# Performance work log

Measured on AMD Instinct MI355X. Metric: run time of the kernel, lower is better.

The kernel has to match this reference:

```python
import jax, jax.numpy as jnp
import numpy as np

B, T, L = 64, 256, 64          # batch, time steps, num_links
H = 128                        # hidden_size
E = 524288                     # num edges
N = B * T                      # nodes seen by GCNConv
IN = L + L * L                 # 4160: concat of link features + flattened distance matrix
OUT = 12 * L                   # fc output size
NUM_LSTM = 2


def setup_inputs() -> dict:
    key = jax.random.key(0)
    ks = jax.random.split(key, 24)
    inp = {
        "x": jax.random.normal(ks[0], (B, T, L), jnp.float32),
        "distance": jax.random.uniform(ks[1], (L, L), jnp.float32),
        "edge_index": jax.random.randint(ks[2], (2, E), 0, N, jnp.int64),
    }
    # GCN layer params (PyG GCNConv: lin weight [in,out] acting as x @ W, bias after aggregation)
    dims = [IN, H, H, H]
    for i in range(3):
        s = 1.0 / np.sqrt(dims[i])
        inp[f"gcn_W{i}"] = jax.random.normal(ks[3 + 2 * i], (dims[i], H), jnp.float32) * s
        inp[f"gcn_b{i}"] = jnp.zeros((H,), jnp.float32)
    # LSTM params, torch layout: W_ih [4H, Hin], W_hh [4H, H], gate order i,f,g,o
    s = 1.0 / np.sqrt(H)
    for l in range(NUM_LSTM):
        inp[f"Wih{l}"] = jax.random.normal(ks[10 + 4 * l], (4 * H, H), jnp.float32) * s
        inp[f"Whh{l}"] = jax.random.normal(ks[11 + 4 * l], (4 * H, H), jnp.float32) * s
        inp[f"bih{l}"] = jax.random.normal(ks[12 + 4 * l], (4 * H,), jnp.float32) * s
        inp[f"bhh{l}"] = jax.random.normal(ks[13 + 4 * l], (4 * H,), jnp.float32) * s
    inp["fc_W"] = jax.random.normal(ks[20], (OUT, H), jnp.float32) * s
    inp["fc_b"] = jnp.zeros((OUT,), jnp.float32)
    return inp


def _gcn(x, W, b, src, dst):
    # GCNConv with add_self_loops=True: out = D^-1/2 (A+I) D^-1/2 (x W) + b
    h = x @ W
    deg = jnp.ones((N,), h.dtype).at[dst].add(1.0)  # in-degree + self loop
    dinv = jax.lax.rsqrt(deg)
    norm = dinv[src] * dinv[dst]                    # [E]
    agg = jnp.zeros_like(h).at[dst].add(h[src] * norm[:, None])
    agg = agg + h * (dinv * dinv)[:, None]          # self-loop term
    return agg + b


def _lstm_layer(xs, Wih, Whh, bih, bhh):
    # xs: [T, B, Hin]
    bias = bih + bhh

    def step(carry, xt):
        h, c = carry
        g = xt @ Wih.T + h @ Whh.T + bias
        i, f, gg, o = jnp.split(g, 4, axis=-1)
        c = jax.nn.sigmoid(f) * c + jax.nn.sigmoid(i) * jnp.tanh(gg)
        h = jax.nn.sigmoid(o) * jnp.tanh(c)
        return (h, c), h

    h0 = jnp.zeros((xs.shape[1], H), xs.dtype)
    _, ys = jax.lax.scan(step, (h0, h0), xs)
    return ys


def reference(x, distance, gcn_W0, gcn_b0, gcn_W1, gcn_b1, gcn_W2, gcn_b2,
              Wih0, Whh0, bih0, bhh0, Wih1, Whh1, bih1, bhh1, fc_W, fc_b,
              edge_index):
    src, dst = edge_index[0], edge_index[1]
    xf = x.reshape(N, L)
    dist_flat = jnp.broadcast_to(distance.reshape(1, L * L), (N, L * L))
    feat = jnp.concatenate([xf, dist_flat], axis=1)  # [N, IN]
    for W, b in ((gcn_W0, gcn_b0), (gcn_W1, gcn_b1), (gcn_W2, gcn_b2)):
        feat = jax.nn.relu(_gcn(feat, W, b, src, dst))
    seq = feat.reshape(B, T, H).transpose(1, 0, 2)   # [T, B, H]
    seq = _lstm_layer(seq, Wih0, Whh0, bih0, bhh0)
    seq = _lstm_layer(seq, Wih1, Whh1, bih1, bhh1)
    last = seq[-1]                                   # [B, H]
    out = last @ fc_W.T + fc_b                       # [B, OUT]
    return out.reshape(B, 12, L)
```

## Files before the change

kernel.cpp:

```cpp
#include <hip/hip_runtime.h>
#include <hip/hip_bf16.h>
#include <cstdint>
#include <cstddef>

#define NB 64
#define NT 256
#define NL 64
#define NH 128
#define NN 16384
#define NE 524288
#define NG 512
#define NOUT 768


__global__ __launch_bounds__(256) void k_transpose(const float* __restrict__ W,
                                                   float* __restrict__ Wt,
                                                   int K, int Nout) {
  int i = blockIdx.x * 256 + threadIdx.x;
  if (i < K * Nout) {
    int k = i / Nout, n = i % Nout;
    Wt[n * K + k] = W[i];
  }
}

__global__ __launch_bounds__(256) void k_dvec(const float* __restrict__ dist,
                                              const float* __restrict__ W0,
                                              float* __restrict__ dvec) {
  __shared__ float red[256];
  int j = blockIdx.x;
  int t = threadIdx.x;
  float acc = 0.f;
  for (int m = t; m < 4096; m += 256)
    acc += dist[m] * W0[(size_t)(64 + m) * 128 + j];
  red[t] = acc;
  __syncthreads();
  for (int off = 128; off > 0; off >>= 1) {
    if (t < off) red[t] += red[t + off];
    __syncthreads();
  }
  if (t == 0) dvec[j] = red[0];
}

__global__ __launch_bounds__(256) void k_count(const int* __restrict__ dst,
                                               int* __restrict__ counts) {
  int i = blockIdx.x * 256 + threadIdx.x;
  atomicAdd(&counts[dst[i]], 1);
}

__global__ __launch_bounds__(256) void k_dinv(const int* __restrict__ counts,
                                              float* __restrict__ dinv) {
  int n = blockIdx.x * 256 + threadIdx.x;
  dinv[n] = rsqrtf((float)counts[n] + 1.0f);
}

__global__ __launch_bounds__(1024) void k_scan(const int* __restrict__ counts,
                                               int* __restrict__ rowstart) {
  __shared__ int part[1024];
  int t = threadIdx.x;
  int base = t * 16;
  int local[16];
  int s = 0;
#pragma unroll
  for (int i = 0; i < 16; i++) { local[i] = s; s += counts[base + i]; }
  part[t] = s;
  __syncthreads();
  for (int off = 1; off < 1024; off <<= 1) {
    int v = (t >= off) ? part[t - off] : 0;
    __syncthreads();
    part[t] += v;
    __syncthreads();
  }
  int prefix = (t == 0) ? 0 : part[t - 1];
#pragma unroll
  for (int i = 0; i < 16; i++) rowstart[base + i] = prefix + local[i];
  if (t == 1023) rowstart[16384] = part[1023];
}

__global__ __launch_bounds__(256) void k_fill(const int* __restrict__ src,
                                              const int* __restrict__ dst,
                                              const int* __restrict__ rowstart,
                                              int* __restrict__ fill,
                                              const float* __restrict__ dinv,
                                              int2* __restrict__ csr) {
  int e = blockIdx.x * 256 + threadIdx.x;
  int sN = src[e], dN = dst[e];
  int pos = rowstart[dN] + atomicAdd(&fill[dN], 1);
  csr[pos] = make_int2(sN, __float_as_int(dinv[sN] * dinv[dN]));
}

template <int K, bool RELU, bool PERMC = false>
__global__ __launch_bounds__(256) void k_gemm_abt(const float* __restrict__ A,
                                                  const float* __restrict__ Bm,
                                                  const float* __restrict__ bias0,
                                                  const float* __restrict__ bias1,
                                                  float* __restrict__ C, int Nn) {
  __shared__ float As[64][K];
  __shared__ float Bs[64][K];
  const int tid = threadIdx.x;
  const int bm = blockIdx.x, bn = blockIdx.y;
  const int VPR = K / 4;
  for (int i = tid; i < 64 * VPR; i += 256) {
    int r = i / VPR, c = i % VPR;
    int xr = (r >> 2) & 7;
    float4 q = *(const float4*)(A + (size_t)(bm * 64 + r) * K + c * 4);
    *(float4*)&As[r][(c ^ xr) * 4] = q;
  }
  for (int i = tid; i < 64 * VPR; i += 256) {
    int r = i / VPR, c = i % VPR;
    int xr = (r >> 2) & 7;
    float4 q = *(const float4*)(Bm + (size_t)(bn * 64 + r) * K + c * 4);
    *(float4*)&Bs[r][(c ^ xr) * 4] = q;
  }
  __syncthreads();
  const int tr = (tid >> 4) << 2;
  const int tc = (tid & 15) << 2;
  const int axor = (tr >> 2) & 7;
  const int bxor = (tc >> 2) & 7;
  float acc[4][4] = {};
#pragma unroll 2
  for (int k4 = 0; k4 < VPR; k4++) {
    int ka = (k4 ^ axor) * 4;
    int kb = (k4 ^ bxor) * 4;
    float4 a0 = *(const float4*)&As[tr + 0][ka];
    float4 a1 = *(const float4*)&As[tr + 1][ka];
    float4 a2 = *(const float4*)&As[tr + 2][ka];
    float4 a3 = *(const float4*)&As[tr + 3][ka];
    float4 b0 = *(const float4*)&Bs[tc + 0][kb];
    float4 b1 = *(const float4*)&Bs[tc + 1][kb];
    float4 b2 = *(const float4*)&Bs[tc + 2][kb];
    float4 b3 = *(const float4*)&Bs[tc + 3][kb];
#define DOT4(i2, j2, av, bv)                                                   \
    acc[i2][j2] = fmaf(av.x, bv.x, acc[i2][j2]);                               \
    acc[i2][j2] = fmaf(av.y, bv.y, acc[i2][j2]);                               \
    acc[i2][j2] = fmaf(av.z, bv.z, acc[i2][j2]);                               \
    acc[i2][j2] = fmaf(av.w, bv.w, acc[i2][j2]);
    DOT4(0, 0, a0, b0) DOT4(0, 1, a0, b1) DOT4(0, 2, a0, b2) DOT4(0, 3, a0, b3)
    DOT4(1, 0, a1, b0) DOT4(1, 1, a1, b1) DOT4(1, 2, a1, b2) DOT4(1, 3, a1, b3)
    DOT4(2, 0, a2, b0) DOT4(2, 1, a2, b1) DOT4(2, 2, a2, b2) DOT4(2, 3, a2, b3)
    DOT4(3, 0, a3, b0) DOT4(3, 1, a3, b1) DOT4(3, 2, a3, b2) DOT4(3, 3, a3, b3)
#undef DOT4
  }
#pragma unroll
  for (int i2 = 0; i2 < 4; i2++) {
    int row = bm * 64 + tr + i2;
#pragma unroll
    for (int j2 = 0; j2 < 4; j2++) {
      int col = bn * 64 + tc + j2;
      float v = acc[i2][j2];
      if (bias0) v += bias0[col];
      if (bias1) v += bias1[col];
      if (RELU) v = fmaxf(v, 0.f);
      int colw = PERMC ? ((col & 127) * 4 + (col >> 7)) : col;
      C[(size_t)row * Nn + colw] = v;
    }
  }
}

__global__ __launch_bounds__(256) void k_agg(const float* __restrict__ h,
                                             const int* __restrict__ rowstart,
                                             const int2* __restrict__ csr,
                                             const float* __restrict__ dinv,
                                             const float* __restrict__ bias,
                                             float* __restrict__ out) {
  int node = blockIdx.x * 4 + (threadIdx.x >> 6);
  int lane = threadIdx.x & 63;
  int s = rowstart[node], e = rowstart[node + 1];
  const float2* h2 = (const float2*)h;
  float ax = 0.f, ay = 0.f;
  int p = s;
  for (; p + 3 < e; p += 4) {
    int2 pk0 = csr[p];
    int2 pk1 = csr[p + 1];
    int2 pk2 = csr[p + 2];
    int2 pk3 = csr[p + 3];
    float2 hv0 = h2[(size_t)pk0.x * 64 + lane];
    float2 hv1 = h2[(size_t)pk1.x * 64 + lane];
    float2 hv2 = h2[(size_t)pk2.x * 64 + lane];
    float2 hv3 = h2[(size_t)pk3.x * 64 + lane];
    float w0 = __int_as_float(pk0.y);
    float w1 = __int_as_float(pk1.y);
    float w2 = __int_as_float(pk2.y);
    float w3 = __int_as_float(pk3.y);
    ax = fmaf(hv0.x, w0, ax); ay = fmaf(hv0.y, w0, ay);
    ax = fmaf(hv1.x, w1, ax); ay = fmaf(hv1.y, w1, ay);
    ax = fmaf(hv2.x, w2, ax); ay = fmaf(hv2.y, w2, ay);
    ax = fmaf(hv3.x, w3, ax); ay = fmaf(hv3.y, w3, ay);
  }
  for (; p < e; p++) {
    int2 pk0 = csr[p];
    float2 hv0 = h2[(size_t)pk0.x * 64 + lane];
    float w0 = __int_as_float(pk0.y);
    ax = fmaf(hv0.x, w0, ax); ay = fmaf(hv0.y, w0, ay);
  }
  float di = dinv[node];
  float sw = di * di;
  float2 hs = h2[(size_t)node * 64 + lane];
  float2 bv = ((const float2*)bias)[lane];
  ax = fmaf(hs.x, sw, ax) + bv.x;
  ay = fmaf(hs.y, sw, ay) + bv.y;
  float2 o;
  o.x = fmaxf(ax, 0.f);
  o.y = fmaxf(ay, 0.f);
  ((float2*)out)[(size_t)node * 64 + lane] = o;
}


template <int CTRL>
__device__ __forceinline__ float dppadd(float x) {
  int r = __builtin_amdgcn_update_dpp(0, __float_as_int(x), CTRL, 0xF, 0xF, true);
  return x + __int_as_float(r);
}

__device__ __forceinline__ float sigf(float x) {
  return 1.f / (1.f + __expf(-x));
}
__device__ __forceinline__ float tanhf_fast(float x) {
  return 1.f - 2.f / (__expf(2.f * x) + 1.f);
}

typedef float f4v __attribute__((ext_vector_type(4)));

template <bool LAST_ONLY>
__global__ __launch_bounds__(512)
__attribute__((amdgpu_waves_per_eu(2, 2)))
void k_lstm7(const float* __restrict__ pre,
             const float* __restrict__ Whh,
             float* __restrict__ yout) {
  __shared__ float hbuf[2][128];
  const int tid = threadIdx.x;
  const int b = blockIdx.x;
  const int c4 = tid & 3;
  const int u = tid >> 2;

  int hidx[8];
#pragma unroll
  for (int j = 0; j < 8; j++) hidx[j] = c4 * 8 + (((u & 7) + 2 * c4 + j) & 7);

#define DECLW(g, j) \
  f4v W##g##_##j = *(const f4v*)(Whh + (size_t)((g)*128 + u) * 128 + hidx[j] * 4);
#define DECLW_ROW(g) \
  DECLW(g, 0) DECLW(g, 1) DECLW(g, 2) DECLW(g, 3) \
  DECLW(g, 4) DECLW(g, 5) DECLW(g, 6) DECLW(g, 7)
  DECLW_ROW(0) DECLW_ROW(1) DECLW_ROW(2) DECLW_ROW(3)
#undef DECLW_ROW
#undef DECLW

  if (tid < 128) hbuf[0][tid] = 0.f;
  float cs = 0.f;
  const float* preb = pre + (size_t)b * NT * NG + tid;
  float pcur = preb[0];
  float* ybase = LAST_ONLY ? (yout + (size_t)b * NH + u)
                           : (yout + (size_t)b * NT * NH + u);
  __syncthreads();

#define PINW(g) \
  asm volatile("" : "+v"(W##g##_0), "+v"(W##g##_1), "+v"(W##g##_2), "+v"(W##g##_3)); \
  asm volatile("" : "+v"(W##g##_4), "+v"(W##g##_5), "+v"(W##g##_6), "+v"(W##g##_7));

#define FMA_J(j)                                                               \
  {                                                                            \
    f4v hv = hp[hidx[j]];                                                      \
    a0 = __builtin_elementwise_fma(W0_##j, hv, a0);                            \
    a1 = __builtin_elementwise_fma(W1_##j, hv, a1);                            \
    a2 = __builtin_elementwise_fma(W2_##j, hv, a2);                            \
    a3 = __builtin_elementwise_fma(W3_##j, hv, a3);                            \
  }

#define LSTM_STEP(CUR, NXT, T)                                                 \
  {                                                                            \
    int tn = (T) + 1; if (tn > NT - 1) tn = NT - 1;                            \
    float pnext = preb[(size_t)tn * NG];                                       \
    const f4v* hp = (const f4v*)&hbuf[CUR][0];                                 \
    f4v a0 = {0.f, 0.f, 0.f, 0.f}, a1 = a0, a2 = a0, a3 = a0;                  \
    FMA_J(0) FMA_J(1) FMA_J(2) FMA_J(3)                                        \
    FMA_J(4) FMA_J(5) FMA_J(6) FMA_J(7)                                        \
    float s0 = (a0.x + a0.y) + (a0.z + a0.w) + ((c4 == 0) ? pcur : 0.f);       \
    float s1 = (a1.x + a1.y) + (a1.z + a1.w) + ((c4 == 1) ? pcur : 0.f);       \
    float s2 = (a2.x + a2.y) + (a2.z + a2.w) + ((c4 == 2) ? pcur : 0.f);       \
    float s3 = (a3.x + a3.y) + (a3.z + a3.w) + ((c4 == 3) ? pcur : 0.f);       \
    s0 = dppadd<0xB1>(s0); s0 = dppadd<0x4E>(s0);                              \
    s1 = dppadd<0xB1>(s1); s1 = dppadd<0x4E>(s1);                              \
    s2 = dppadd<0xB1>(s2); s2 = dppadd<0x4E>(s2);                              \
    s3 = dppadd<0xB1>(s3); s3 = dppadd<0x4E>(s3);                              \
    float si = sigf(s0), sf = sigf(s1), tg = tanhf_fast(s2), so = sigf(s3);    \
    cs = sf * cs + si * tg;                                                    \
    float hnew = so * tanhf_fast(cs);                                          \
    if (c4 == 0) hbuf[NXT][u] = hnew;                                          \
    if (!LAST_ONLY) {                                                          \
      if (c4 == 1) ybase[(size_t)(T) * NH] = hnew;                             \
    } else if ((T) == NT - 1) {                                                \
      if (c4 == 1) *ybase = hnew;                                              \
    }                                                                          \
    pcur = pnext;                                                              \
    __syncthreads();                                                           \
  }

  for (int t = 0; t < NT; t += 2) {
    PINW(0) PINW(1) PINW(2) PINW(3)
    LSTM_STEP(0, 1, t);
    LSTM_STEP(1, 0, t + 1);
  }
#undef LSTM_STEP
#undef FMA_J
#undef PINW
}


extern "C" void kernel_launch(void* const* d_in, const int* in_sizes, int n_in,
                              void* d_out, int out_size, void* d_ws, size_t ws_size,
                              hipStream_t stream) {
  const float* x    = (const float*)d_in[0];
  const float* dist = (const float*)d_in[1];
  const int*   ei   = (const int*)d_in[2];
  const float* W0   = (const float*)d_in[3];
  const float* b0   = (const float*)d_in[4];
  const float* W1   = (const float*)d_in[5];
  const float* b1   = (const float*)d_in[6];
  const float* W2   = (const float*)d_in[7];
  const float* b2   = (const float*)d_in[8];
  const float* Wih0 = (const float*)d_in[9];
  const float* Whh0 = (const float*)d_in[10];
  const float* bih0 = (const float*)d_in[11];
  const float* bhh0 = (const float*)d_in[12];
  const float* Wih1 = (const float*)d_in[13];
  const float* Whh1 = (const float*)d_in[14];
  const float* bih1 = (const float*)d_in[15];
  const float* bhh1 = (const float*)d_in[16];
  const float* fcW  = (const float*)d_in[17];
  const float* fcb  = (const float*)d_in[18];
  float* out = (float*)d_out;

  char* ws = (char*)d_ws;
  size_t off = 0;
  auto alloc = [&](size_t bytes) -> void* {
    void* p = ws + off;
    off += (bytes + 255) & ~(size_t)255;
    return p;
  };
  float* bufA     = (float*)alloc((size_t)NN * 128 * 4);
  float* bufB     = (float*)alloc((size_t)NN * 128 * 4);
  float* pre      = (float*)alloc((size_t)NN * 512 * 4);
  int2*  csr      = (int2*)alloc((size_t)NE * 8);
  int*   counts   = (int*)alloc((size_t)NN * 4);
  int*   fillc    = (int*)alloc((size_t)NN * 4);
  int*   rowstart = (int*)alloc((size_t)(NN + 1) * 4);
  float* dinv     = (float*)alloc((size_t)NN * 4);
  float* dvec     = (float*)alloc(128 * 4);
  float* hlast    = (float*)alloc(64 * 128 * 4);
  float* wt0      = (float*)alloc(128 * 64 * 4);
  float* wt1      = (float*)alloc(128 * 128 * 4);
  float* wt2      = (float*)alloc(128 * 128 * 4);
  (void)ws_size; (void)in_sizes; (void)n_in; (void)out_size;

  const int* srcIdx = ei;
  const int* dstIdx = ei + NE;

  hipMemsetAsync(counts, 0, (size_t)NN * 4, stream);
  hipMemsetAsync(fillc, 0, (size_t)NN * 4, stream);

  k_transpose<<<(64 * 128 + 255) / 256, 256, 0, stream>>>(W0, wt0, 64, 128);
  k_transpose<<<(128 * 128 + 255) / 256, 256, 0, stream>>>(W1, wt1, 128, 128);
  k_transpose<<<(128 * 128 + 255) / 256, 256, 0, stream>>>(W2, wt2, 128, 128);
  k_dvec<<<128, 256, 0, stream>>>(dist, W0, dvec);

  k_count<<<NE / 256, 256, 0, stream>>>(dstIdx, counts);
  k_scan<<<1, 1024, 0, stream>>>(counts, rowstart);
  k_dinv<<<NN / 256, 256, 0, stream>>>(counts, dinv);
  k_fill<<<NE / 256, 256, 0, stream>>>(srcIdx, dstIdx, rowstart, fillc, dinv, csr);

  dim3 gH(NN / 64, 128 / 64);
  k_gemm_abt<64, false><<<gH, 256, 0, stream>>>(x, wt0, dvec, nullptr, bufB, 128);
  k_agg<<<NN / 4, 256, 0, stream>>>(bufB, rowstart, csr, dinv, b0, bufA);
  k_gemm_abt<128, false><<<gH, 256, 0, stream>>>(bufA, wt1, nullptr, nullptr, bufB, 128);
  k_agg<<<NN / 4, 256, 0, stream>>>(bufB, rowstart, csr, dinv, b1, bufA);
  k_gemm_abt<128, false><<<gH, 256, 0, stream>>>(bufA, wt2, nullptr, nullptr, bufB, 128);
  k_agg<<<NN / 4, 256, 0, stream>>>(bufB, rowstart, csr, dinv, b2, bufA);

  dim3 gP(NN / 64, 512 / 64);
  k_gemm_abt<128, false, true><<<gP, 256, 0, stream>>>(bufA, Wih0, bih0, bhh0, pre, 512);
  k_lstm7<false><<<64, 512, 0, stream>>>(pre, Whh0, bufB);
  k_gemm_abt<128, false, true><<<gP, 256, 0, stream>>>(bufB, Wih1, bih1, bhh1, pre, 512);
  k_lstm7<true><<<64, 512, 0, stream>>>(pre, Whh1, hlast);

  dim3 gF(1, NOUT / 64);
  k_gemm_abt<128, false><<<gF, 256, 0, stream>>>(hlast, fcW, fcb, nullptr, out, NOUT);
}
```

Measured before the change: 823.0 us.

## Move half of LSTM recurrent weights to LDS as packed bf16, fuse dinv into scan

The LSTM recurrence kernel previously held all four gates' recurrent weights in VGPRs. It now keeps only the g and o gate weights in registers. The i and f gate weights are pre-packed to bf16 by a new kernel and staged into 64KB of dynamic LDS, then read and unpacked each step. This cuts register pressure, at the cost of extra LDS traffic per step and reduced precision on two gates. Separately, the dinv computation is folded into the scan kernel to drop one launch.

```diff
diff --git a/kernel.cpp b/kernel.cpp
--- a/kernel.cpp
+++ b/kernel.cpp
@@ -47,21 +47,20 @@
   atomicAdd(&counts[dst[i]], 1);
 }
 
-__global__ __launch_bounds__(256) void k_dinv(const int* __restrict__ counts,
-                                              float* __restrict__ dinv) {
-  int n = blockIdx.x * 256 + threadIdx.x;
-  dinv[n] = rsqrtf((float)counts[n] + 1.0f);
-}
-
 __global__ __launch_bounds__(1024) void k_scan(const int* __restrict__ counts,
-                                               int* __restrict__ rowstart) {
+                                               int* __restrict__ rowstart,
+                                               float* __restrict__ dinv) {
   __shared__ int part[1024];
   int t = threadIdx.x;
   int base = t * 16;
   int local[16];
   int s = 0;
 #pragma unroll
-  for (int i = 0; i < 16; i++) { local[i] = s; s += counts[base + i]; }
+  for (int i = 0; i < 16; i++) {
+    int cv = counts[base + i];
+    local[i] = s; s += cv;
+    dinv[base + i] = rsqrtf((float)cv + 1.0f);
+  }
   part[t] = s;
   __syncthreads();
   for (int off = 1; off < 1024; off <<= 1) {
@@ -86,6 +85,30 @@
   int sN = src[e], dN = dst[e];
   int pos = rowstart[dN] + atomicAdd(&fill[dN], 1);
   csr[pos] = make_int2(sN, __float_as_int(dinv[sN] * dinv[dN]));
+}
+
+__device__ __forceinline__ unsigned rne_bf16(float f) {
+  unsigned u = __float_as_uint(f);
+  return (u + 0x7FFFu + ((u >> 16) & 1u)) >> 16;
+}
+
+__global__ __launch_bounds__(256) void k_packw2(const float* __restrict__ Whh,
+                                                uint4* __restrict__ out) {
+  int idx = blockIdx.x * 256 + threadIdx.x;
+  int c = idx >> 9, tid = idx & 511;
+  int u = tid >> 2, c4 = tid & 3;
+  int g = c >> 2, q = c & 3;
+  int h0 = c4 * 8 + (((u & 7) + 2 * c4 + 2 * q) & 7);
+  int h1 = c4 * 8 + (((u & 7) + 2 * c4 + 2 * q + 1) & 7);
+  const float* row = Whh + (size_t)(g * 128 + u) * 128;
+  const float* p0 = row + h0 * 4;
+  const float* p1 = row + h1 * 4;
+  uint4 o;
+  o.x = rne_bf16(p0[0]) | (rne_bf16(p0[1]) << 16);
+  o.y = rne_bf16(p0[2]) | (rne_bf16(p0[3]) << 16);
+  o.z = rne_bf16(p1[0]) | (rne_bf16(p1[1]) << 16);
+  o.w = rne_bf16(p1[2]) | (rne_bf16(p1[3]) << 16);
+  out[c * 512 + tid] = o;
 }
 
 template <int K, bool RELU, bool PERMC = false>
@@ -218,15 +241,31 @@
   return 1.f - 2.f / (__expf(2.f * x) + 1.f);
 }
 
+typedef float f2v __attribute__((ext_vector_type(2)));
 typedef float f4v __attribute__((ext_vector_type(4)));
+
+__device__ __forceinline__ f2v unpk(unsigned d) {
+  f2v r;
+  r.x = __uint_as_float(d << 16);
+  r.y = __uint_as_float(d & 0xFFFF0000u);
+  return r;
+}
+__device__ __forceinline__ f2v mk2(float a, float b) {
+  f2v r; r.x = a; r.y = b; return r;
+}
+
+#define LSTM11_SHBYTES (65536 + 1024)
 
 template <bool LAST_ONLY>
 __global__ __launch_bounds__(512)
 __attribute__((amdgpu_waves_per_eu(2, 2)))
-void k_lstm7(const float* __restrict__ pre,
-             const float* __restrict__ Whh,
-             float* __restrict__ yout) {
-  __shared__ float hbuf[2][128];
+void k_lstm11(const float* __restrict__ pre,
+              const float* __restrict__ Whh,
+              const uint4* __restrict__ wpkA,
+              float* __restrict__ yout) {
+  extern __shared__ unsigned char smem[];
+  uint4* wlds = (uint4*)smem;
+  float* hb   = (float*)(smem + 65536);
   const int tid = threadIdx.x;
   const int b = blockIdx.x;
   const int c4 = tid & 3;
@@ -236,16 +275,18 @@
 #pragma unroll
   for (int j = 0; j < 8; j++) hidx[j] = c4 * 8 + (((u & 7) + 2 * c4 + j) & 7);
 
+#pragma unroll
+  for (int c = 0; c < 8; c++) wlds[c * 512 + tid] = wpkA[c * 512 + tid];
+
 #define DECLW(g, j) \
   f4v W##g##_##j = *(const f4v*)(Whh + (size_t)((g)*128 + u) * 128 + hidx[j] * 4);
-#define DECLW_ROW(g) \
-  DECLW(g, 0) DECLW(g, 1) DECLW(g, 2) DECLW(g, 3) \
-  DECLW(g, 4) DECLW(g, 5) DECLW(g, 6) DECLW(g, 7)
-  DECLW_ROW(0) DECLW_ROW(1) DECLW_ROW(2) DECLW_ROW(3)
-#undef DECLW_ROW
+  DECLW(2, 0) DECLW(2, 1) DECLW(2, 2) DECLW(2, 3)
+  DECLW(2, 4) DECLW(2, 5) DECLW(2, 6) DECLW(2, 7)
+  DECLW(3, 0) DECLW(3, 1) DECLW(3, 2) DECLW(3, 3)
+  DECLW(3, 4) DECLW(3, 5) DECLW(3, 6) DECLW(3, 7)
 #undef DECLW
 
-  if (tid < 128) hbuf[0][tid] = 0.f;
+  if (tid < 128) hb[tid] = 0.f;
   float cs = 0.f;
   const float* preb = pre + (size_t)b * NT * NG + tid;
   float pcur = preb[0];
@@ -257,27 +298,48 @@
   asm volatile("" : "+v"(W##g##_0), "+v"(W##g##_1), "+v"(W##g##_2), "+v"(W##g##_3)); \
   asm volatile("" : "+v"(W##g##_4), "+v"(W##g##_5), "+v"(W##g##_6), "+v"(W##g##_7));
 
+#define GATEL(g, SG)                                                           \
+  {                                                                            \
+    f2v ag = {0.f, 0.f};                                                       \
+    _Pragma("unroll")                                                          \
+    for (int q = 0; q < 4; q++) {                                              \
+      uint4 wd = wlds[((g) * 4 + q) * 512 + tid];                              \
+      f4v ha = hv[2 * q];                                                      \
+      f4v hc = hv[2 * q + 1];                                                  \
+      ag = __builtin_elementwise_fma(unpk(wd.x), mk2(ha.x, ha.y), ag);         \
+      ag = __builtin_elementwise_fma(unpk(wd.y), mk2(ha.z, ha.w), ag);         \
+      ag = __builtin_elementwise_fma(unpk(wd.z), mk2(hc.x, hc.y), ag);         \
+      ag = __builtin_elementwise_fma(unpk(wd.w), mk2(hc.z, hc.w), ag);         \
+    }                                                                          \
+    SG = ag.x + ag.y;                                                          \
+  }
+
 #define FMA_J(j)                                                               \
   {                                                                            \
-    f4v hv = hp[hidx[j]];                                                      \
-    a0 = __builtin_elementwise_fma(W0_##j, hv, a0);                            \
-    a1 = __builtin_elementwise_fma(W1_##j, hv, a1);                            \
-    a2 = __builtin_elementwise_fma(W2_##j, hv, a2);                            \
-    a3 = __builtin_elementwise_fma(W3_##j, hv, a3);                            \
+    f4v hj = hv[j];                                                            \
+    a2 = __builtin_elementwise_fma(W2_##j, hj, a2);                            \
+    a3 = __builtin_elementwise_fma(W3_##j, hj, a3);                            \
   }
 
 #define LSTM_STEP(CUR, NXT, T)                                                 \
   {                                                                            \
     int tn = (T) + 1; if (tn > NT - 1) tn = NT - 1;                            \
     float pnext = preb[(size_t)tn * NG];                                       \
-    const f4v* hp = (const f4v*)&hbuf[CUR][0];                                 \
-    f4v a0 = {0.f, 0.f, 0.f, 0.f}, a1 = a0, a2 = a0, a3 = a0;                  \
+    const f4v* hp = (const f4v*)(hb + (CUR) * 128);                            \
+    f4v hv[8];                                                                 \
+    _Pragma("unroll")                                                          \
+    for (int j = 0; j < 8; j++) hv[j] = hp[hidx[j]];                           \
+    float s0, s1;                                                              \
+    GATEL(0, s0) GATEL(1, s1)                                                  \
+    f4v a2 = {0.f, 0.f, 0.f, 0.f}, a3 = a2;                                    \
     FMA_J(0) FMA_J(1) FMA_J(2) FMA_J(3)                                        \
     FMA_J(4) FMA_J(5) FMA_J(6) FMA_J(7)                                        \
-    float s0 = (a0.x + a0.y) + (a0.z + a0.w) + ((c4 == 0) ? pcur : 0.f);       \
-    float s1 = (a1.x + a1.y) + (a1.z + a1.w) + ((c4 == 1) ? pcur : 0.f);       \
-    float s2 = (a2.x + a2.y) + (a2.z + a2.w) + ((c4 == 2) ? pcur : 0.f);       \
-    float s3 = (a3.x + a3.y) + (a3.z + a3.w) + ((c4 == 3) ? pcur : 0.f);       \
+    float s2 = (a2.x + a2.y) + (a2.z + a2.w);                                  \
+    float s3 = (a3.x + a3.y) + (a3.z + a3.w);                                  \
+    s0 += (c4 == 0) ? pcur : 0.f;                                              \
+    s1 += (c4 == 1) ? pcur : 0.f;                                              \
+    s2 += (c4 == 2) ? pcur : 0.f;                                              \
+    s3 += (c4 == 3) ? pcur : 0.f;                                              \
     s0 = dppadd<0xB1>(s0); s0 = dppadd<0x4E>(s0);                              \
     s1 = dppadd<0xB1>(s1); s1 = dppadd<0x4E>(s1);                              \
     s2 = dppadd<0xB1>(s2); s2 = dppadd<0x4E>(s2);                              \
@@ -285,7 +347,7 @@
     float si = sigf(s0), sf = sigf(s1), tg = tanhf_fast(s2), so = sigf(s3);    \
     cs = sf * cs + si * tg;                                                    \
     float hnew = so * tanhf_fast(cs);                                          \
-    if (c4 == 0) hbuf[NXT][u] = hnew;                                          \
+    if (c4 == 0) hb[(NXT) * 128 + u] = hnew;                                   \
     if (!LAST_ONLY) {                                                          \
       if (c4 == 1) ybase[(size_t)(T) * NH] = hnew;                             \
     } else if ((T) == NT - 1) {                                                \
@@ -296,12 +358,13 @@
   }
 
   for (int t = 0; t < NT; t += 2) {
-    PINW(0) PINW(1) PINW(2) PINW(3)
+    PINW(2) PINW(3)
     LSTM_STEP(0, 1, t);
     LSTM_STEP(1, 0, t + 1);
   }
 #undef LSTM_STEP
 #undef FMA_J
+#undef GATEL
 #undef PINW
 }
 
@@ -350,6 +413,8 @@
   float* wt0      = (float*)alloc(128 * 64 * 4);
   float* wt1      = (float*)alloc(128 * 128 * 4);
   float* wt2      = (float*)alloc(128 * 128 * 4);
+  uint4* wpkA0    = (uint4*)alloc((size_t)4096 * 16);
+  uint4* wpkA1    = (uint4*)alloc((size_t)4096 * 16);
   (void)ws_size; (void)in_sizes; (void)n_in; (void)out_size;
 
   const int* srcIdx = ei;
@@ -357,15 +422,21 @@
 
   hipMemsetAsync(counts, 0, (size_t)NN * 4, stream);
   hipMemsetAsync(fillc, 0, (size_t)NN * 4, stream);
+
+  hipFuncSetAttribute(reinterpret_cast<const void*>(&k_lstm11<false>),
+                      hipFuncAttributeMaxDynamicSharedMemorySize, LSTM11_SHBYTES);
+  hipFuncSetAttribute(reinterpret_cast<const void*>(&k_lstm11<true>),
+                      hipFuncAttributeMaxDynamicSharedMemorySize, LSTM11_SHBYTES);
 
   k_transpose<<<(64 * 128 + 255) / 256, 256, 0, stream>>>(W0, wt0, 64, 128);
   k_transpose<<<(128 * 128 + 255) / 256, 256, 0, stream>>>(W1, wt1, 128, 128);
   k_transpose<<<(128 * 128 + 255) / 256, 256, 0, stream>>>(W2, wt2, 128, 128);
   k_dvec<<<128, 256, 0, stream>>>(dist, W0, dvec);
+  k_packw2<<<16, 256, 0, stream>>>(Whh0, wpkA0);
+  k_packw2<<<16, 256, 0, stream>>>(Whh1, wpkA1);
 
   k_count<<<NE / 256, 256, 0, stream>>>(dstIdx, counts);
-  k_scan<<<1, 1024, 0, stream>>>(counts, rowstart);
-  k_dinv<<<NN / 256, 256, 0, stream>>>(counts, dinv);
+  k_scan<<<1, 1024, 0, stream>>>(counts, rowstart, dinv);
   k_fill<<<NE / 256, 256, 0, stream>>>(srcIdx, dstIdx, rowstart, fillc, dinv, csr);
 
   dim3 gH(NN / 64, 128 / 64);
@@ -378,9 +449,9 @@
 
   dim3 gP(NN / 64, 512 / 64);
   k_gemm_abt<128, false, true><<<gP, 256, 0, stream>>>(bufA, Wih0, bih0, bhh0, pre, 512);
-  k_lstm7<false><<<64, 512, 0, stream>>>(pre, Whh0, bufB);
+  k_lstm11<false><<<64, 512, LSTM11_SHBYTES, stream>>>(pre, Whh0, wpkA0, bufB);
   k_gemm_abt<128, false, true><<<gP, 256, 0, stream>>>(bufB, Wih1, bih1, bhh1, pre, 512);
-  k_lstm7<true><<<64, 512, 0, stream>>>(pre, Whh1, hlast);
+  k_lstm11<true><<<64, 512, LSTM11_SHBYTES, stream>>>(pre, Whh1, wpkA1, hlast);
 
   dim3 gF(1, NOUT / 64);
   k_gemm_abt<128, false><<<gF, 256, 0, stream>>>(hlast, fcW, fcb, nullptr, out, NOUT);
```

New measurement: 940.6 us. 14.3% more time.
